# Optimization experiments

Hardware: AMD Instinct MI355X
Metric: run time of the kernel (lower is better)

Reference implementation:

```python
import jax, jax.numpy as jnp
import numpy as np

L_IN, L_FREQ, L_OUT = 128, 64, 64
C_IN, C_OUT, T_DIM = 64, 64, 256
SPIN = 1

# ---------- self-contained spin-weighted SHT (MW sampling), replacing s2fft ----------

def _mw_thetas(L, extended):
    n = 2 * L - 1 if extended else L
    return (2 * np.arange(n) + 1) * np.pi / (2 * L - 1)

def _wigner_d_stack(L, thetas, n):
    # d^l_{m,n}(theta) = <l,m| exp(-i theta Jy) |l,n>, computed via eigh of the
    # Hermitian angular-momentum operator Jy. Output (ntheta, L, 2L-1), m at col L-1+m.
    nth = len(thetas)
    out = np.zeros((nth, L, 2 * L - 1), dtype=np.float64)
    for l in range(abs(n), L):
        dim = 2 * l + 1
        m = np.arange(-l, l).astype(np.float64)
        ap = np.sqrt(l * (l + 1.0) - m * (m + 1.0))
        Jy = np.zeros((dim, dim), dtype=np.complex128)
        i = np.arange(dim - 1)
        Jy[i + 1, i] = -0.5j * ap
        Jy[i, i + 1] = 0.5j * ap
        lam, V = np.linalg.eigh(Jy)
        coeff = V * np.conj(V[l + n, :])[None, :]
        phases = np.exp(-1j * np.outer(lam, thetas))
        out[:, l, L - 1 - l:L + l] = (coeff @ phases).T.real
    return out

def _mw_quad_weights(L):
    # per-theta weights on the mirror-extended grid: q_t = (1/(2L-1)) sum_k w(k) e^{ik theta_t}
    # with w(k) = int_0^pi e^{ik t} sin(t) dt
    k = np.arange(-(L - 1), L)
    den = np.where(np.abs(k) == 1, 1, 1 - k * k).astype(np.float64)
    w = np.where(k % 2 == 0, 2.0 / den, 0.0).astype(np.complex128)
    w[k == 1] = 0.5j * np.pi
    w[k == -1] = -0.5j * np.pi
    th = _mw_thetas(L, True)
    return ((w[None, :] * np.exp(1j * np.outer(th, k))).sum(1) / (2 * L - 1)).real

# transform kernels are constants (built once at import, numpy)
_D_FWD = jnp.asarray(_wigner_d_stack(L_IN, _mw_thetas(L_IN, True), -SPIN) * _mw_quad_weights(L_IN)[:, None, None], jnp.float32)
_D_INV = jnp.asarray(_wigner_d_stack(L_OUT, _mw_thetas(L_OUT, False), -SPIN), jnp.float32)
_CL_IN = jnp.asarray(((-1.0) ** SPIN) * np.sqrt((2 * np.arange(L_IN) + 1) / (4 * np.pi)), jnp.float32)
_CL_OUT = jnp.asarray(((-1.0) ** SPIN) * np.sqrt((2 * np.arange(L_OUT) + 1) / (4 * np.pi)), jnp.float32)
_m_all = np.arange(-(L_IN - 1), L_IN)
_PARITY = jnp.asarray(np.where((_m_all + SPIN) % 2 == 0, 1.0, -1.0), jnp.float32)

def sht_forward(x):
    # x: (L_IN, 2*L_IN-1, C) real spatial -> flm: (L_IN, 2*L_IN-1, C) complex, m at L_IN-1+m
    nphi = 2 * L_IN - 1
    ftm = jnp.fft.fftshift(jnp.fft.fft(x, axis=1), axes=1) * (2 * jnp.pi / nphi)
    # mirror extension in theta with (-1)^(m+spin) parity (all channels at once)
    g_ext = jnp.concatenate([ftm, _PARITY[None, :, None] * ftm[::-1][1:]], axis=0)
    flm = jnp.einsum('tlm,tmc->lmc', _D_FWD, g_ext)
    return flm * _CL_IN[:, None, None]

def sht_inverse(flm):
    # flm: (L_OUT, 2*L_OUT-1, C) complex -> (L_OUT, 2*L_OUT-1, C) real spatial
    ftm = jnp.einsum('tlm,lmc->tmc', _D_INV, flm * _CL_OUT[:, None, None])
    return (jnp.fft.ifft(jnp.fft.ifftshift(ftm, axes=1), axis=1) * (2 * L_OUT - 1)).real

def resize_flm(flm, l_in, l_out):
    # centered truncation / zero-pad of (L, 2L-1, C) harmonic coefficients
    if l_out <= l_in:
        d = l_in - l_out
        return flm[:l_out, d:d + 2 * l_out - 1]
    d = l_out - l_in
    return jnp.pad(flm, ((0, d), (d, d), (0, 0)))

# ---------- inputs and parameters ----------

def setup_inputs():
    key = jax.random.key(0)
    ks = jax.random.split(key, 12)
    n = lambda i, shape, s: jax.random.normal(ks[i], shape, jnp.float32) * s
    return {
        'x': jax.random.normal(ks[0], (L_IN, 2 * L_IN - 1, C_IN), jnp.float32),
        't_emb': jax.random.normal(ks[1], (T_DIM,), jnp.float32),
        'spec_conv_w': n(2, (C_IN, C_OUT), (1.0 / C_IN) ** 0.5),
        'spec_conv_b': jnp.zeros((C_OUT,), jnp.float32),
        'spec_wr': n(3, (L_FREQ, C_IN, C_OUT), (0.5 / C_IN) ** 0.5),
        'spec_wi': n(4, (L_FREQ, C_IN, C_OUT), (0.5 / C_IN) ** 0.5),
        'spec_tr_w': n(5, (T_DIM, L_FREQ), (1.0 / T_DIM) ** 0.5),
        'spec_tr_b': jnp.zeros((L_FREQ,), jnp.float32),
        'spec_ti_w': n(6, (T_DIM, L_FREQ), (1.0 / T_DIM) ** 0.5),
        'spec_ti_b': jnp.zeros((L_FREQ,), jnp.float32),
        'spat_conv1_w': n(7, (C_IN, C_OUT), (1.0 / C_IN) ** 0.5),
        'spat_conv1_b': jnp.zeros((C_OUT,), jnp.float32),
        'spat_t_w': n(8, (T_DIM, 2 * C_OUT), (1.0 / T_DIM) ** 0.5),
        'spat_t_b': jnp.zeros((2 * C_OUT,), jnp.float32),
        'spat_weight': n(9, (C_OUT, C_OUT), 0.01),
        'spat_conv2_w': n(10, (C_OUT, C_OUT), (1.0 / C_OUT) ** 0.5),
        'spat_conv2_b': jnp.zeros((C_OUT,), jnp.float32),
        'ln_scale': jnp.ones((C_OUT,), jnp.float32),
        'ln_bias': jnp.zeros((C_OUT,), jnp.float32),
    }

def reference(x, t_emb, spec_conv_w, spec_conv_b, spec_wr, spec_wi, spec_tr_w, spec_tr_b, spec_ti_w, spec_ti_b, spat_conv1_w, spat_conv1_b, spat_t_w, spat_t_b, spat_weight, spat_conv2_w, spat_conv2_b, ln_scale, ln_bias):
    # ----- SphericalSpectralTimeConv branch -----
    flm = sht_forward(x)                                   # (L_IN, 2L_IN-1, C_IN) complex
    flm = resize_flm(flm, L_IN, L_FREQ)                    # (L_FREQ, 2L_FREQ-1, C_IN)
    conv_flm = jnp.einsum('lmi,io->lmo', flm, spec_conv_w) + spec_conv_b
    t_c = (t_emb @ spec_tr_w + spec_tr_b) + 1j * (t_emb @ spec_ti_w + spec_ti_b)   # (L_FREQ,)
    w = t_c[:, None, None] * (spec_wr + 1j * spec_wi)      # (L_FREQ, C_IN, C_OUT)
    flm = jnp.einsum('lmi,lio->lmo', flm, w) + conv_flm
    xs = sht_inverse(resize_flm(flm, L_FREQ, L_OUT))       # (L_OUT, 2L_OUT-1, C_OUT) real
    xs = xs / (jnp.linalg.norm(xs, axis=-1, keepdims=True) + 1e-6)
    # ----- SpatialTimeConv branch (path='down') -----
    h = jnp.einsum('lmi,io->lmo', x, spat_conv1_w) + spat_conv1_b
    t = t_emb @ spat_t_w + spat_t_b
    w_t, b_t = t[:C_OUT], t[C_OUT:]
    h = jnp.einsum('lmi,io->lmo', h, w_t[None, :] * spat_weight)
    h = sht_inverse(resize_flm(sht_forward(h), L_IN, L_OUT))
    h = jnp.einsum('lmi,io->lmo', h, spat_conv2_w) + spat_conv2_b + b_t
    # ----- combine: add, gelu, LayerNorm (eps=1e-6 over channels) -----
    y = jax.nn.gelu(xs + h)
    mu = jnp.mean(y, axis=-1, keepdims=True)
    var = jnp.var(y, axis=-1, keepdims=True)
    return (y - mu) * jax.lax.rsqrt(var + 1e-6) * ln_scale + ln_bias
```

## Files before the change

### kernel.cpp

```cpp
#include <hip/hip_runtime.h>
#include <math.h>

#define DPI 3.141592653589793238462643383279502884

__device__ __forceinline__ float wave_sum64(float v) {
#pragma unroll
  for (int off = 32; off > 0; off >>= 1) v += __shfl_xor(v, off, 64);
  return v;
}

__device__ __forceinline__ float gelu_tanh(float v) {
  float u = 0.7978845608028654f * (v + 0.044715f * v * v * v);
  return 0.5f * v * (1.0f + tanhf(u));
}

#define CN255F ((float)(-2.0 * DPI / 255.0))
#define CN127F ((float)(2.0 * DPI / 127.0))
#define PIO255F ((float)(DPI / 255.0))


__device__ __forceinline__ void dft_block(int t, int tid, const float* __restrict__ x,
                                          float* __restrict__ ftm_re, float* __restrict__ ftm_im,
                                          char* sm) {
  float* xs_ = (float*)sm;
  int cg_ = tid & 15, mg = tid >> 4;
  float wr[4], wi[4], rc[4], rs[4];
#pragma unroll
  for (int j = 0; j < 4; ++j) {
    int m = mg * 4 + j;
    __sincosf(CN255F * (float)m, &rs[j], &rc[j]);
    wr[j] = 1.0f; wi[j] = 0.0f;
  }
  float accr[4][4], acci[4][4];
#pragma unroll
  for (int j = 0; j < 4; ++j)
#pragma unroll
    for (int q = 0; q < 4; ++q) { accr[j][q] = 0.f; acci[j][q] = 0.f; }
  for (int k0 = 0; k0 < 255; k0 += 64) {
    int kn = (255 - k0 < 64) ? 255 - k0 : 64;
    __syncthreads();
    {
      const float4* src = (const float4*)(x + ((size_t)t * 255 + k0) * 64);
      float4* dst = (float4*)xs_;
      int lim = kn * 16;
#pragma unroll
      for (int q = 0; q < 4; ++q) {
        int fidx = tid + q * 256;
        if (fidx < lim) dst[fidx] = src[fidx];
      }
    }
    __syncthreads();
#pragma unroll 2
    for (int k = 0; k < kn; ++k) {
      float4 xv = *(const float4*)&xs_[k * 64 + cg_ * 4];
      float xv4[4] = {xv.x, xv.y, xv.z, xv.w};
#pragma unroll
      for (int j = 0; j < 4; ++j) {
#pragma unroll
        for (int q = 0; q < 4; ++q) {
          accr[j][q] = fmaf(xv4[q], wr[j], accr[j][q]);
          acci[j][q] = fmaf(xv4[q], wi[j], acci[j][q]);
        }
        float nw = wr[j] * rc[j] - wi[j] * rs[j];
        wi[j] = fmaf(wr[j], rs[j], wi[j] * rc[j]);
        wr[j] = nw;
      }
    }
  }
#pragma unroll
  for (int j = 0; j < 4; ++j) {
    int mi = mg * 4 + j;
    size_t ob = ((size_t)t * 64 + mi) * 64 + cg_ * 4;
    *(float4*)(ftm_re + ob) = make_float4(accr[j][0], accr[j][1], accr[j][2], accr[j][3]);
    *(float4*)(ftm_im + ob) = make_float4(acci[j][0], acci[j][1], acci[j][2], acci[j][3]);
  }
}

__device__ __forceinline__ void wigner_block(int wb, int tid, float* __restrict__ Deff,
                                             float* __restrict__ Dinv, char* sm) {
  float* LF = (float*)sm;
  float* red = (float*)(sm + 512);
  float* clf = (float*)(sm + 1024);
  int mode = (wb < 128) ? 0 : 1;
  int t, mm;
  if (mode == 0) { t = wb; mm = tid; }
  else { mm = wb - 128; t = (tid < 64) ? tid : 63; }
  if (tid < 64) clf[tid] = (float)(-sqrt((2.0 * tid + 1.0) / (4.0 * DPI)));
  if (tid < 128) LF[tid] = (tid == 0) ? 0.f : logf((float)tid);
  __syncthreads();
  for (int s = 1; s < 128; s <<= 1) {
    float add = (tid < 128 && tid >= s) ? LF[tid - s] : 0.f;
    __syncthreads();
    if (tid < 128) LF[tid] += add;
    __syncthreads();
  }
  float coeff = 1.0f;
  int odd = 2 * t + 1;
  if (mode == 0) {
    if (tid < 63) {
      int k = 2 * (tid + 1);
      int e = (k * odd) % 510;
      float ang = (float)e * PIO255F;
      red[tid] = 8.0f * __cosf(ang) / (1.0f - (float)(k * k));
    } else if (tid == 63) {
      red[63] = 4.0f;
    }
    __syncthreads();
    for (int s = 32; s > 0; s >>= 1) {
      if (tid < s) red[tid] += red[tid + s];
      __syncthreads();
    }
    float s = red[0] / 255.0f;
    if (t == 127) s *= 0.5f;
    coeff = s * (float)(2.0 * DPI / 255.0);
  }
  bool active = (mode == 0) ? (tid < 127) : (tid < 64);
  if (!active) return;
  int m = mm - 63;
  double denomN = (mode == 0) ? 255.0 : 127.0;
  double beta = (double)odd * DPI / denomN;
  double chd, shd;
  sincos(0.5 * beta, &shd, &chd);
  float cbf = (float)cos(beta);
  float chf = (float)chd, shf = (float)shd;
  int am = (m < 0) ? -m : m;
  int l0v = (am > 1) ? am : 1;
  float seed;
  if (m == 0) {
    seed = -1.4142135623730951f * shf * chf;
  } else {
    int j = am;
    float lch = logf(chf), lsh = logf(shf);
    float e0 = 0.5f * (LF[2 * j] - LF[j - 1] - LF[j + 1]);
    float expo = (m >= 1) ? e0 + (float)(j - 1) * lch + (float)(j + 1) * lsh
                          : e0 + (float)(j + 1) * lch + (float)(j - 1) * lsh;
    float sv = __expf(expo);
    seed = (m >= 1 && ((m + 1) & 1)) ? -sv : sv;
  }
  float dl = seed, dm1 = 0.0f, S_cur = 0.0f;
  float mf = (float)m;
  for (int l = 0; l < 64; ++l) {
    float val = 0.0f;
    if (l >= l0v) {
      val = dl * coeff * clf[l];
      float Ld = (float)l, lp = Ld + 1.0f;
      float S_next = sqrtf((lp * lp - mf * mf) * (lp * lp - 1.0f));
      float num1 = (2.0f * Ld + 1.0f) * (Ld * lp * cbf + mf);
      float dn = (num1 * dl - lp * S_cur * dm1) / (Ld * S_next);
      dm1 = dl; dl = dn; S_cur = S_next;
    }
    if (mode == 0) Deff[((size_t)t * 127 + mm) * 64 + l] = val;
    else Dinv[((size_t)mm * 64 + l) * 64 + t] = val;
  }
}

__device__ __forceinline__ void a2_block(int l, int tid, const float* __restrict__ temb,
                                         const float* __restrict__ trw, const float* __restrict__ trb,
                                         const float* __restrict__ tiw, const float* __restrict__ tib,
                                         const float* __restrict__ scw, const float* __restrict__ swr,
                                         const float* __restrict__ swi, float2* __restrict__ A2,
                                         char* sm) {
  float* fb1 = (float*)sm;
  float* fb2 = (float*)(sm + 1024);
  fb1[tid] = temb[tid] * trw[tid * 64 + l];
  fb2[tid] = temb[tid] * tiw[tid * 64 + l];
  __syncthreads();
  for (int s = 128; s > 0; s >>= 1) {
    if (tid < s) { fb1[tid] += fb1[tid + s]; fb2[tid] += fb2[tid + s]; }
    __syncthreads();
  }
  float tr = fb1[0] + trb[l], ti = fb2[0] + tib[l];
  int o = tid & 63, iq = tid >> 6;
  for (int i = iq * 16; i < iq * 16 + 16; ++i) {
    int idx = (l * 64 + i) * 64 + o;
    float r = swr[idx], s2 = swi[idx];
    A2[idx] = make_float2(scw[i * 64 + o] + tr * r - ti * s2, tr * s2 + ti * r);
  }
}

__device__ __forceinline__ void m_block(int j, int tid, const float* __restrict__ temb,
                                        const float* __restrict__ stw, const float* __restrict__ stb,
                                        const float* __restrict__ c1w, const float* __restrict__ c1b,
                                        const float* __restrict__ sweight, float* __restrict__ Mm,
                                        float* __restrict__ bias2, char* sm) {
  float* fb1 = (float*)sm;
  float* fb2 = (float*)(sm + 1024);
  int o = tid & 63, part = tid >> 6;
  float p = 0.f;
  for (int k = part * 64; k < part * 64 + 64; ++k)
    p = fmaf(temb[k], stw[k * 128 + o], p);
  fb1[part * 64 + o] = p;
  __syncthreads();
  if (part == 0) fb2[o] = fb1[o] + fb1[64 + o] + fb1[128 + o] + fb1[192 + o] + stb[o];
  __syncthreads();
  float tvo = fb2[o];
  float q = 0.f;
  for (int i = part * 16; i < part * 16 + 16; ++i)
    q = fmaf(c1w[j * 64 + i], sweight[i * 64 + o], q);
  __syncthreads();
  fb1[part * 64 + o] = q;
  __syncthreads();
  if (part == 0) Mm[j * 64 + o] = tvo * (fb1[o] + fb1[64 + o] + fb1[128 + o] + fb1[192 + o]);
  if (j == 0) {
    float bq = 0.f;
    for (int i = part * 16; i < part * 16 + 16; ++i)
      bq = fmaf(c1b[i], sweight[i * 64 + o], bq);
    __syncthreads();
    fb1[part * 64 + o] = bq;
    __syncthreads();
    if (part == 0) bias2[o] = tvo * (fb1[o] + fb1[64 + o] + fb1[128 + o] + fb1[192 + o]);
  }
}

__device__ __forceinline__ void tv_block(int tid, const float* __restrict__ temb,
                                         const float* __restrict__ stw, const float* __restrict__ stb,
                                         float* __restrict__ tv, char* sm) {
  float* fb1 = (float*)sm;
  int o = tid & 127, part = tid >> 7;
  float p = 0.f;
  for (int k = part * 128; k < part * 128 + 128; ++k)
    p = fmaf(temb[k], stw[k * 128 + o], p);
  fb1[part * 128 + o] = p;
  __syncthreads();
  if (part == 0) tv[o] = fb1[o] + fb1[128 + o] + stb[o];
}

__global__ __launch_bounds__(256) void ct_pre(
    const float* __restrict__ x, const float* __restrict__ temb,
    const float* __restrict__ trw, const float* __restrict__ trb,
    const float* __restrict__ tiw, const float* __restrict__ tib,
    const float* __restrict__ stw, const float* __restrict__ stb,
    const float* __restrict__ scw, const float* __restrict__ swr,
    const float* __restrict__ swi, const float* __restrict__ c1w,
    const float* __restrict__ c1b, const float* __restrict__ sweight,
    float* __restrict__ Deff, float* __restrict__ Dinv,
    float2* __restrict__ A2, float* __restrict__ Mm,
    float* __restrict__ bias2, float* __restrict__ tv,
    float* __restrict__ ftm_re, float* __restrict__ ftm_im) {
  __shared__ __align__(16) char sm[16384];
  int vb = blockIdx.x;
  int tid = threadIdx.x;
  if (vb < 128) dft_block(vb, tid, x, ftm_re, ftm_im, sm);
  else if (vb < 383) wigner_block(vb - 128, tid, Deff, Dinv, sm);
  else if (vb < 447) a2_block(vb - 383, tid, temb, trw, trb, tiw, tib, scw, swr, swi, A2, sm);
  else if (vb < 511) m_block(vb - 447, tid, temb, stw, stb, c1w, c1b, sweight, Mm, bias2, sm);
  else tv_block(tid, temb, stw, stb, tv, sm);
}

__global__ __launch_bounds__(256) void ct_projf(const float* __restrict__ Deff,
                                                const float* __restrict__ ftm_re,
                                                const float* __restrict__ ftm_im,
                                                float* __restrict__ flm_re,
                                                float* __restrict__ flm_im) {
  __shared__ float Dsh[64][32];
  __shared__ float fr_[64][64], fi_[64][64];
  int mm = blockIdx.x, lh = blockIdx.y;
  int mi = (mm >= 63) ? (mm - 63) : (63 - mm);
  float csign = (mm >= 63) ? 1.0f : -1.0f;
  int tid = threadIdx.x;
  int cg_ = tid & 15, lg = tid >> 4;
  float ar[2][4], ai[2][4];
#pragma unroll
  for (int li = 0; li < 2; ++li)
#pragma unroll
    for (int q = 0; q < 4; ++q) { ar[li][q] = 0.f; ai[li][q] = 0.f; }
  for (int th2 = 0; th2 < 2; ++th2) {
    int tb = th2 * 64;
    __syncthreads();
    for (int e = tid; e < 64 * 32; e += 256) {
      int r = e >> 5, li = e & 31;
      Dsh[r][li] = Deff[((size_t)(tb + r) * 127 + mm) * 64 + lh * 32 + li];
    }
    for (int e = tid; e < 64 * 64; e += 256) {
      int r = e >> 6, c = e & 63;
      size_t idx = ((size_t)(tb + r) * 64 + mi) * 64 + c;
      fr_[r][c] = ftm_re[idx];
      fi_[r][c] = csign * ftm_im[idx];
    }
    __syncthreads();
#pragma unroll 4
    for (int k = 0; k < 64; ++k) {
      float4 fr4 = *(const float4*)&fr_[k][cg_ * 4];
      float4 fi4 = *(const float4*)&fi_[k][cg_ * 4];
      float2 d2 = *(const float2*)&Dsh[k][lg * 2];
      float frv[4] = {fr4.x, fr4.y, fr4.z, fr4.w};
      float fiv[4] = {fi4.x, fi4.y, fi4.z, fi4.w};
      float dv[2] = {d2.x, d2.y};
#pragma unroll
      for (int li = 0; li < 2; ++li)
#pragma unroll
        for (int q = 0; q < 4; ++q) {
          ar[li][q] = fmaf(dv[li], frv[q], ar[li][q]);
          ai[li][q] = fmaf(dv[li], fiv[q], ai[li][q]);
        }
    }
  }
#pragma unroll
  for (int li = 0; li < 2; ++li) {
    size_t row = ((size_t)mm * 64 + lh * 32 + lg * 2 + li) * 64 + cg_ * 4;
    *(float4*)(flm_re + row) = make_float4(ar[li][0], ar[li][1], ar[li][2], ar[li][3]);
    *(float4*)(flm_im + row) = make_float4(ai[li][0], ai[li][1], ai[li][2], ai[li][3]);
  }
}

__global__ __launch_bounds__(256) void ct_mix(const float* __restrict__ flm_re,
                                              const float* __restrict__ flm_im,
                                              const float2* __restrict__ A2,
                                              const float* __restrict__ Mm,
                                              const float* __restrict__ scb,
                                              const float* __restrict__ bias2,
                                              const float* __restrict__ Deff,
                                              float* __restrict__ s_re, float* __restrict__ s_im,
                                              float* __restrict__ h_re, float* __restrict__ h_im) {
  __shared__ float Ar_[64][32], Ai_[64][32], Msh[64][32];
  __shared__ float Br_[64][65], Bi_[64][65];
  __shared__ float rb[256];
  int l = blockIdx.x, mh = blockIdx.y, oh = blockIdx.z;
  int tid = threadIdx.x;
  int og = tid & 15, mg = tid >> 4;
  rb[tid] = (mh == 0 && tid < 128) ? Deff[((size_t)tid * 127 + 63) * 64 + l] : 0.f;
  __syncthreads();
  for (int s = 128; s > 0; s >>= 1) {
    if (tid < s) rb[tid] += rb[tid + s];
    __syncthreads();
  }
  float slv = rb[0];
  for (int e = tid; e < 64 * 32; e += 256) {
    int r = e >> 5, oi = e & 31;
    float2 aa = A2[((size_t)l * 64 + r) * 64 + oh * 32 + oi];
    Ar_[r][oi] = aa.x; Ai_[r][oi] = aa.y;
    Msh[r][oi] = Mm[r * 64 + oh * 32 + oi];
  }
  for (int e = tid; e < 64 * 64; e += 256) {
    int mi = e >> 6, i = e & 63;
    int gmm = mh * 64 + mi; if (gmm > 126) gmm = 126;
    size_t idx = ((size_t)gmm * 64 + l) * 64 + i;
    Br_[mi][i] = flm_re[idx];
    Bi_[mi][i] = flm_im[idx];
  }
  __syncthreads();
  int o0 = oh * 32 + og * 2;
  float b0[2] = {scb[o0], scb[o0 + 1]};
  float sr[4][2], si[4][2], hr[4][2], hi[4][2];
#pragma unroll
  for (int jm = 0; jm < 4; ++jm)
#pragma unroll
    for (int qo = 0; qo < 2; ++qo) {
      sr[jm][qo] = b0[qo]; si[jm][qo] = 0.f; hr[jm][qo] = 0.f; hi[jm][qo] = 0.f;
    }
#pragma unroll 4
  for (int k = 0; k < 64; ++k) {
    float2 ar2 = *(const float2*)&Ar_[k][og * 2];
    float2 ai2 = *(const float2*)&Ai_[k][og * 2];
    float2 mv2 = *(const float2*)&Msh[k][og * 2];
    float br4[4], bi4[4];
#pragma unroll
    for (int jm = 0; jm < 4; ++jm) {
      br4[jm] = Br_[mg * 4 + jm][k];
      bi4[jm] = Bi_[mg * 4 + jm][k];
    }
    float arv[2] = {ar2.x, ar2.y}, aiv[2] = {ai2.x, ai2.y}, mvv[2] = {mv2.x, mv2.y};
#pragma unroll
    for (int jm = 0; jm < 4; ++jm)
#pragma unroll
      for (int qo = 0; qo < 2; ++qo) {
        sr[jm][qo] = fmaf(br4[jm], arv[qo], sr[jm][qo]);
        sr[jm][qo] = fmaf(-bi4[jm], aiv[qo], sr[jm][qo]);
        si[jm][qo] = fmaf(br4[jm], aiv[qo], si[jm][qo]);
        si[jm][qo] = fmaf(bi4[jm], arv[qo], si[jm][qo]);
        hr[jm][qo] = fmaf(br4[jm], mvv[qo], hr[jm][qo]);
        hi[jm][qo] = fmaf(bi4[jm], mvv[qo], hi[jm][qo]);
      }
  }
  float bb[2] = {bias2[o0], bias2[o0 + 1]};
#pragma unroll
  for (int jm = 0; jm < 4; ++jm) {
    int gmm = mh * 64 + mg * 4 + jm;
    if (gmm > 126) continue;
    if (gmm == 63) {
#pragma unroll
      for (int qo = 0; qo < 2; ++qo)
        hr[jm][qo] = fmaf(255.0f * slv, bb[qo], hr[jm][qo]);
    }
    size_t row = ((size_t)gmm * 64 + l) * 64 + o0;
    *(float2*)(s_re + row) = make_float2(sr[jm][0], sr[jm][1]);
    *(float2*)(s_im + row) = make_float2(si[jm][0], si[jm][1]);
    *(float2*)(h_re + row) = make_float2(hr[jm][0], hr[jm][1]);
    *(float2*)(h_im + row) = make_float2(hi[jm][0], hi[jm][1]);
  }
}

__global__ __launch_bounds__(256) void ct_proji(const float* __restrict__ Dinv,
                                                const float* __restrict__ s_re,
                                                const float* __restrict__ s_im,
                                                const float* __restrict__ h_re,
                                                const float* __restrict__ h_im,
                                                float* __restrict__ fos_re, float* __restrict__ fos_im,
                                                float* __restrict__ foh_re, float* __restrict__ foh_im) {
  __shared__ float Dsh[64][64];
  __shared__ float Br_[64][32], Bi_[64][32];
  int mm = blockIdx.x, br = blockIdx.y, ch = blockIdx.z;
  const float* ire = br ? h_re : s_re;
  const float* iim = br ? h_im : s_im;
  float* ore = br ? foh_re : fos_re;
  float* oim = br ? foh_im : fos_im;
  int tid = threadIdx.x;
  int cg_ = tid & 15, tg = tid >> 4;
  for (int e = tid; e < 64 * 64; e += 256) {
    int r = e >> 6, tt = e & 63;
    Dsh[r][tt] = Dinv[((size_t)mm * 64 + r) * 64 + tt];
  }
  for (int e = tid; e < 64 * 32; e += 256) {
    int r = e >> 5, cc = e & 31;
    size_t idx = ((size_t)mm * 64 + r) * 64 + ch * 32 + cc;
    Br_[r][cc] = ire[idx];
    Bi_[r][cc] = iim[idx];
  }
  __syncthreads();
  float ar[4][2], ai[4][2];
#pragma unroll
  for (int j = 0; j < 4; ++j)
#pragma unroll
    for (int q = 0; q < 2; ++q) { ar[j][q] = 0.f; ai[j][q] = 0.f; }
#pragma unroll 4
  for (int k = 0; k < 64; ++k) {
    float4 d4 = *(const float4*)&Dsh[k][tg * 4];
    float2 fr2 = *(const float2*)&Br_[k][cg_ * 2];
    float2 fi2 = *(const float2*)&Bi_[k][cg_ * 2];
    float dv[4] = {d4.x, d4.y, d4.z, d4.w};
    float frv[2] = {fr2.x, fr2.y}, fiv[2] = {fi2.x, fi2.y};
#pragma unroll
    for (int j = 0; j < 4; ++j)
#pragma unroll
      for (int q = 0; q < 2; ++q) {
        ar[j][q] = fmaf(dv[j], frv[q], ar[j][q]);
        ai[j][q] = fmaf(dv[j], fiv[q], ai[j][q]);
      }
  }
#pragma unroll
  for (int j = 0; j < 4; ++j) {
    int t = tg * 4 + j;
    size_t ob = ((size_t)t * 127 + mm) * 64 + ch * 32 + cg_ * 2;
    *(float2*)(ore + ob) = make_float2(ar[j][0], ar[j][1]);
    *(float2*)(oim + ob) = make_float2(ai[j][0], ai[j][1]);
  }
}

__global__ __launch_bounds__(256) void ct_idft(const float* __restrict__ fos_re,
                                               const float* __restrict__ fos_im,
                                               const float* __restrict__ foh_re,
                                               const float* __restrict__ foh_im,
                                               float* __restrict__ xsb, float* __restrict__ hsb) {
  __shared__ float Br_[32][64], Bi_[32][64];
  int t = blockIdx.x, br = blockIdx.y, ph = blockIdx.z;
  const float* fre = br ? foh_re : fos_re;
  const float* fim = br ? foh_im : fos_im;
  float* outp = br ? hsb : xsb;
  int tid = threadIdx.x;
  int cg_ = tid & 15, pg = tid >> 4;
  float wc[4], ws[4], rc[4], rs[4];
#pragma unroll
  for (int j = 0; j < 4; ++j) {
    int gp = ph * 64 + pg * 4 + j; if (gp > 126) gp = 126;
    __sincosf(CN127F * (float)gp, &rs[j], &rc[j]);
    int r0 = (-63 * gp) % 127;
    __sincosf(CN127F * (float)r0, &ws[j], &wc[j]);
  }
  float acc[4][4];
#pragma unroll
  for (int j = 0; j < 4; ++j)
#pragma unroll
    for (int q = 0; q < 4; ++q) acc[j][q] = 0.f;
  for (int k0 = 0; k0 < 127; k0 += 32) {
    int kn = (127 - k0 < 32) ? 127 - k0 : 32;
    __syncthreads();
    for (int e = tid; e < 32 * 64; e += 256) {
      int r = e >> 6, j = e & 63;
      if (r < kn) {
        size_t bidx = ((size_t)t * 127 + k0 + r) * 64 + j;
        Br_[r][j] = fre[bidx]; Bi_[r][j] = fim[bidx];
      }
    }
    __syncthreads();
#pragma unroll 2
    for (int k = 0; k < kn; ++k) {
      float4 b_r = *(const float4*)&Br_[k][cg_ * 4];
      float4 b_i = *(const float4*)&Bi_[k][cg_ * 4];
      float brv[4] = {b_r.x, b_r.y, b_r.z, b_r.w};
      float biv[4] = {b_i.x, b_i.y, b_i.z, b_i.w};
#pragma unroll
      for (int j = 0; j < 4; ++j) {
#pragma unroll
        for (int q = 0; q < 4; ++q) {
          acc[j][q] = fmaf(brv[q], wc[j], acc[j][q]);
          acc[j][q] = fmaf(biv[q], -ws[j], acc[j][q]);
        }
        float nw = wc[j] * rc[j] - ws[j] * rs[j];
        ws[j] = fmaf(wc[j], rs[j], ws[j] * rc[j]);
        wc[j] = nw;
      }
    }
  }
#pragma unroll
  for (int j = 0; j < 4; ++j) {
    int gp = ph * 64 + pg * 4 + j;
    if (gp > 126) continue;
    *(float4*)(outp + ((size_t)t * 127 + gp) * 64 + cg_ * 4) =
        make_float4(acc[j][0], acc[j][1], acc[j][2], acc[j][3]);
  }
}

__global__ __launch_bounds__(256) void ct_fin(const float* __restrict__ xsb,
                                              const float* __restrict__ hsb,
                                              const float* __restrict__ c2w,
                                              const float* __restrict__ c2b,
                                              const float* __restrict__ tv,
                                              const float* __restrict__ lns,
                                              const float* __restrict__ lnb,
                                              float* __restrict__ out) {
  int w = threadIdx.x >> 6, lane = threadIdx.x & 63;
  size_t row = (size_t)blockIdx.x * 4 + w;
  size_t base = row * 64 + lane;
  float hv = hsb[base];
  float xv = xsb[base];
  float acc = c2b[lane] + tv[64 + lane];
#pragma unroll 16
  for (int i = 0; i < 64; ++i)
    acc = fmaf(__shfl(hv, i, 64), c2w[i * 64 + lane], acc);
  float ss = wave_sum64(xv * xv);
  xv = xv / (sqrtf(ss) + 1e-6f);
  float y = xv + acc;
  float g = gelu_tanh(y);
  float mu = wave_sum64(g) * (1.0f / 64.0f);
  float d = g - mu;
  float var = wave_sum64(d * d) * (1.0f / 64.0f);
  out[base] = d * rsqrtf(var + 1e-6f) * lns[lane] + lnb[lane];
}

extern "C" void kernel_launch(void* const* d_in, const int* in_sizes, int n_in,
                              void* d_out, int out_size, void* d_ws, size_t ws_size,
                              hipStream_t stream) {
  const float* x = (const float*)d_in[0];
  const float* temb = (const float*)d_in[1];
  const float* scw = (const float*)d_in[2];
  const float* scb = (const float*)d_in[3];
  const float* swr = (const float*)d_in[4];
  const float* swi = (const float*)d_in[5];
  const float* strw = (const float*)d_in[6];
  const float* strb = (const float*)d_in[7];
  const float* stiw = (const float*)d_in[8];
  const float* stib = (const float*)d_in[9];
  const float* c1w = (const float*)d_in[10];
  const float* c1b = (const float*)d_in[11];
  const float* stw = (const float*)d_in[12];
  const float* stb = (const float*)d_in[13];
  const float* sweight = (const float*)d_in[14];
  const float* c2w = (const float*)d_in[15];
  const float* c2b = (const float*)d_in[16];
  const float* lns = (const float*)d_in[17];
  const float* lnb = (const float*)d_in[18];
  float* out = (float*)d_out;

  char* base = (char*)d_ws;
  size_t off = 0;
  auto alloc = [&](size_t bytes) -> void* {
    void* p = base + off;
    off += (bytes + 255) & ~(size_t)255;
    return p;
  };
  float* tv = (float*)alloc(128 * sizeof(float));
  float* Mm = (float*)alloc(4096 * sizeof(float));
  float* bias2 = (float*)alloc(64 * sizeof(float));
  float2* A2 = (float2*)alloc(262144 * sizeof(float2));
  float* Deff = (float*)alloc(1040384 * sizeof(float));
  float* Dinv = (float*)alloc(520192 * sizeof(float));
  float* ftm_re = (float*)alloc(524288 * sizeof(float));
  float* ftm_im = (float*)alloc(524288 * sizeof(float));
  float* flm_re = (float*)alloc(520192 * sizeof(float));
  float* flm_im = (float*)alloc(520192 * sizeof(float));
  float* s_re = (float*)alloc(520192 * sizeof(float));
  float* s_im = (float*)alloc(520192 * sizeof(float));
  float* h_re = (float*)alloc(520192 * sizeof(float));
  float* h_im = (float*)alloc(520192 * sizeof(float));
  float* fos_re = (float*)alloc(520192 * sizeof(float));
  float* fos_im = (float*)alloc(520192 * sizeof(float));
  float* foh_re = (float*)alloc(520192 * sizeof(float));
  float* foh_im = (float*)alloc(520192 * sizeof(float));
  float* xsb = (float*)alloc(520192 * sizeof(float));
  float* hsb = (float*)alloc(520192 * sizeof(float));
  if (off > ws_size) return;

  hipLaunchKernelGGL(ct_pre, dim3(512), dim3(256), 0, stream,
                     x, temb, strw, strb, stiw, stib, stw, stb,
                     scw, swr, swi, c1w, c1b, sweight,
                     Deff, Dinv, A2, Mm, bias2, tv, ftm_re, ftm_im);
  hipLaunchKernelGGL(ct_projf, dim3(127, 2), dim3(256), 0, stream, Deff,
                     ftm_re, ftm_im, flm_re, flm_im);
  hipLaunchKernelGGL(ct_mix, dim3(64, 2, 2), dim3(256), 0, stream,
                     flm_re, flm_im, A2, Mm, scb, bias2, Deff,
                     s_re, s_im, h_re, h_im);
  hipLaunchKernelGGL(ct_proji, dim3(127, 2, 2), dim3(256), 0, stream, Dinv,
                     s_re, s_im, h_re, h_im, fos_re, fos_im, foh_re, foh_im);
  hipLaunchKernelGGL(ct_idft, dim3(64, 2, 2), dim3(256), 0, stream,
                     fos_re, fos_im, foh_re, foh_im, xsb, hsb);
  hipLaunchKernelGGL(ct_fin, dim3(2032), dim3(256), 0, stream, xsb, hsb,
                     c2w, c2b, tv, lns, lnb, out);
}
```

Baseline: 195.4 us.

## Split DFT blocks across channel halves and software-prefetch LDS operands in inner loops

The DFT stage in the prep kernel now uses twice as many blocks, each covering half the channels for one theta row. This spreads the serial DFT work over more CUs and shortens the critical path of ct_pre. Separately, the inner loops of the DFT, forward projection, inverse projection and inverse DFT kernels now load the next shared-memory operands a step ahead so LDS latency overlaps with FMAs. This replaces the previous unroll pragmas. The cost is extra registers, and the compiler's unrolling may be lost.

```diff
diff --git a/kernel.cpp b/kernel.cpp
--- a/kernel.cpp
+++ b/kernel.cpp
@@ -19,43 +19,44 @@
 #define PIO255F ((float)(DPI / 255.0))
 
 
-__device__ __forceinline__ void dft_block(int t, int tid, const float* __restrict__ x,
+__device__ __forceinline__ void dft_block(int idx, int tid, const float* __restrict__ x,
                                           float* __restrict__ ftm_re, float* __restrict__ ftm_im,
                                           char* sm) {
   float* xs_ = (float*)sm;
-  int cg_ = tid & 15, mg = tid >> 4;
-  float wr[4], wi[4], rc[4], rs[4];
-#pragma unroll
-  for (int j = 0; j < 4; ++j) {
-    int m = mg * 4 + j;
+  int t = idx >> 1, ch = idx & 1;
+  int cbase = ch * 32;
+  int cg_ = tid & 7, mg = tid >> 3;
+  float wr[2], wi[2], rc[2], rs[2];
+#pragma unroll
+  for (int j = 0; j < 2; ++j) {
+    int m = mg * 2 + j;
     __sincosf(CN255F * (float)m, &rs[j], &rc[j]);
     wr[j] = 1.0f; wi[j] = 0.0f;
   }
-  float accr[4][4], acci[4][4];
-#pragma unroll
-  for (int j = 0; j < 4; ++j)
+  float accr[2][4], acci[2][4];
+#pragma unroll
+  for (int j = 0; j < 2; ++j)
 #pragma unroll
     for (int q = 0; q < 4; ++q) { accr[j][q] = 0.f; acci[j][q] = 0.f; }
   for (int k0 = 0; k0 < 255; k0 += 64) {
     int kn = (255 - k0 < 64) ? 255 - k0 : 64;
     __syncthreads();
     {
-      const float4* src = (const float4*)(x + ((size_t)t * 255 + k0) * 64);
-      float4* dst = (float4*)xs_;
-      int lim = kn * 16;
-#pragma unroll
-      for (int q = 0; q < 4; ++q) {
-        int fidx = tid + q * 256;
-        if (fidx < lim) dst[fidx] = src[fidx];
-      }
-    }
-    __syncthreads();
-#pragma unroll 2
+      int lim = kn * 8;
+      for (int f = tid; f < lim; f += 256) {
+        int r = f >> 3, cc = f & 7;
+        ((float4*)xs_)[f] =
+            *(const float4*)(x + ((size_t)t * 255 + k0 + r) * 64 + cbase + cc * 4);
+      }
+    }
+    __syncthreads();
+    float4 cur = *(const float4*)&xs_[0 * 32 + cg_ * 4];
+    float4 nxt = (kn > 1) ? *(const float4*)&xs_[1 * 32 + cg_ * 4] : cur;
     for (int k = 0; k < kn; ++k) {
-      float4 xv = *(const float4*)&xs_[k * 64 + cg_ * 4];
-      float xv4[4] = {xv.x, xv.y, xv.z, xv.w};
-#pragma unroll
-      for (int j = 0; j < 4; ++j) {
+      float4 nn = (k + 2 < kn) ? *(const float4*)&xs_[(k + 2) * 32 + cg_ * 4] : cur;
+      float xv4[4] = {cur.x, cur.y, cur.z, cur.w};
+#pragma unroll
+      for (int j = 0; j < 2; ++j) {
 #pragma unroll
         for (int q = 0; q < 4; ++q) {
           accr[j][q] = fmaf(xv4[q], wr[j], accr[j][q]);
@@ -65,12 +66,13 @@
         wi[j] = fmaf(wr[j], rs[j], wi[j] * rc[j]);
         wr[j] = nw;
       }
-    }
-  }
-#pragma unroll
-  for (int j = 0; j < 4; ++j) {
-    int mi = mg * 4 + j;
-    size_t ob = ((size_t)t * 64 + mi) * 64 + cg_ * 4;
+      cur = nxt; nxt = nn;
+    }
+  }
+#pragma unroll
+  for (int j = 0; j < 2; ++j) {
+    int mi = mg * 2 + j;
+    size_t ob = ((size_t)t * 64 + mi) * 64 + cbase + cg_ * 4;
     *(float4*)(ftm_re + ob) = make_float4(accr[j][0], accr[j][1], accr[j][2], accr[j][3]);
     *(float4*)(ftm_im + ob) = make_float4(acci[j][0], acci[j][1], acci[j][2], acci[j][3]);
   }
@@ -240,10 +242,10 @@
   __shared__ __align__(16) char sm[16384];
   int vb = blockIdx.x;
   int tid = threadIdx.x;
-  if (vb < 128) dft_block(vb, tid, x, ftm_re, ftm_im, sm);
-  else if (vb < 383) wigner_block(vb - 128, tid, Deff, Dinv, sm);
-  else if (vb < 447) a2_block(vb - 383, tid, temb, trw, trb, tiw, tib, scw, swr, swi, A2, sm);
-  else if (vb < 511) m_block(vb - 447, tid, temb, stw, stb, c1w, c1b, sweight, Mm, bias2, sm);
+  if (vb < 256) dft_block(vb, tid, x, ftm_re, ftm_im, sm);
+  else if (vb < 511) wigner_block(vb - 256, tid, Deff, Dinv, sm);
+  else if (vb < 575) a2_block(vb - 511, tid, temb, trw, trb, tiw, tib, scw, swr, swi, A2, sm);
+  else if (vb < 639) m_block(vb - 575, tid, temb, stw, stb, c1w, c1b, sweight, Mm, bias2, sm);
   else tv_block(tid, temb, stw, stb, tv, sm);
 }
 
@@ -278,14 +280,20 @@
       fi_[r][c] = csign * ftm_im[idx];
     }
     __syncthreads();
-#pragma unroll 4
+    float4 cr = *(const float4*)&fr_[0][cg_ * 4];
+    float4 ci = *(const float4*)&fi_[0][cg_ * 4];
+    float2 cd = *(const float2*)&Dsh[0][lg * 2];
     for (int k = 0; k < 64; ++k) {
-      float4 fr4 = *(const float4*)&fr_[k][cg_ * 4];
-      float4 fi4 = *(const float4*)&fi_[k][cg_ * 4];
-      float2 d2 = *(const float2*)&Dsh[k][lg * 2];
-      float frv[4] = {fr4.x, fr4.y, fr4.z, fr4.w};
-      float fiv[4] = {fi4.x, fi4.y, fi4.z, fi4.w};
-      float dv[2] = {d2.x, d2.y};
+      float4 nr = cr, ni = ci;
+      float2 nd = cd;
+      if (k + 1 < 64) {
+        nr = *(const float4*)&fr_[k + 1][cg_ * 4];
+        ni = *(const float4*)&fi_[k + 1][cg_ * 4];
+        nd = *(const float2*)&Dsh[k + 1][lg * 2];
+      }
+      float frv[4] = {cr.x, cr.y, cr.z, cr.w};
+      float fiv[4] = {ci.x, ci.y, ci.z, ci.w};
+      float dv[2] = {cd.x, cd.y};
 #pragma unroll
       for (int li = 0; li < 2; ++li)
 #pragma unroll
@@ -293,6 +301,7 @@
           ar[li][q] = fmaf(dv[li], frv[q], ar[li][q]);
           ai[li][q] = fmaf(dv[li], fiv[q], ai[li][q]);
         }
+      cr = nr; ci = ni; cd = nd;
     }
   }
 #pragma unroll
@@ -422,13 +431,18 @@
   for (int j = 0; j < 4; ++j)
 #pragma unroll
     for (int q = 0; q < 2; ++q) { ar[j][q] = 0.f; ai[j][q] = 0.f; }
-#pragma unroll 4
+  float4 cd = *(const float4*)&Dsh[0][tg * 4];
+  float2 crf = *(const float2*)&Br_[0][cg_ * 2];
+  float2 cif = *(const float2*)&Bi_[0][cg_ * 2];
   for (int k = 0; k < 64; ++k) {
-    float4 d4 = *(const float4*)&Dsh[k][tg * 4];
-    float2 fr2 = *(const float2*)&Br_[k][cg_ * 2];
-    float2 fi2 = *(const float2*)&Bi_[k][cg_ * 2];
-    float dv[4] = {d4.x, d4.y, d4.z, d4.w};
-    float frv[2] = {fr2.x, fr2.y}, fiv[2] = {fi2.x, fi2.y};
+    float4 nd = cd; float2 nrf = crf, nif = cif;
+    if (k + 1 < 64) {
+      nd = *(const float4*)&Dsh[k + 1][tg * 4];
+      nrf = *(const float2*)&Br_[k + 1][cg_ * 2];
+      nif = *(const float2*)&Bi_[k + 1][cg_ * 2];
+    }
+    float dv[4] = {cd.x, cd.y, cd.z, cd.w};
+    float frv[2] = {crf.x, crf.y}, fiv[2] = {cif.x, cif.y};
 #pragma unroll
     for (int j = 0; j < 4; ++j)
 #pragma unroll
@@ -436,6 +450,7 @@
         ar[j][q] = fmaf(dv[j], frv[q], ar[j][q]);
         ai[j][q] = fmaf(dv[j], fiv[q], ai[j][q]);
       }
+    cd = nd; crf = nrf; cif = nif;
   }
 #pragma unroll
   for (int j = 0; j < 4; ++j) {
@@ -482,12 +497,16 @@
       }
     }
     __syncthreads();
-#pragma unroll 2
+    float4 cbr = *(const float4*)&Br_[0][cg_ * 4];
+    float4 cbi = *(const float4*)&Bi_[0][cg_ * 4];
     for (int k = 0; k < kn; ++k) {
-      float4 b_r = *(const float4*)&Br_[k][cg_ * 4];
-      float4 b_i = *(const float4*)&Bi_[k][cg_ * 4];
-      float brv[4] = {b_r.x, b_r.y, b_r.z, b_r.w};
-      float biv[4] = {b_i.x, b_i.y, b_i.z, b_i.w};
+      float4 nbr = cbr, nbi = cbi;
+      if (k + 1 < kn) {
+        nbr = *(const float4*)&Br_[k + 1][cg_ * 4];
+        nbi = *(const float4*)&Bi_[k + 1][cg_ * 4];
+      }
+      float brv[4] = {cbr.x, cbr.y, cbr.z, cbr.w};
+      float biv[4] = {cbi.x, cbi.y, cbi.z, cbi.w};
 #pragma unroll
       for (int j = 0; j < 4; ++j) {
 #pragma unroll
@@ -499,6 +518,7 @@
         ws[j] = fmaf(wc[j], rs[j], ws[j] * rc[j]);
         wc[j] = nw;
       }
+      cbr = nbr; cbi = nbi;
     }
   }
 #pragma unroll
@@ -590,7 +610,7 @@
   float* hsb = (float*)alloc(520192 * sizeof(float));
   if (off > ws_size) return;
 
-  hipLaunchKernelGGL(ct_pre, dim3(512), dim3(256), 0, stream,
+  hipLaunchKernelGGL(ct_pre, dim3(640), dim3(256), 0, stream,
                      x, temb, strw, strb, stiw, stib, stw, stb,
                      scw, swr, swi, c1w, c1b, sweight,
                      Deff, Dinv, A2, Mm, bias2, tv, ftm_re, ftm_im);
```

New measurement: 194.7 us. Within noise of the previous version (-0.4%).
